# Kernel optimization log

Hardware: AMD Instinct MI355X
Metric: run time of the kernel (lower is better)

The kernel has to match this reference:

```python
import jax, jax.numpy as jnp
import numpy as np

B, M, E, K = 8, 256, 128, 16
H, A, R, RMS = 1024, 256, 1024, 512
NEG = -1e25


def setup_inputs() -> dict:
    key = jax.random.key(0)
    ks = jax.random.split(key, 12)
    inp = {
        "mention_reprs": jax.random.normal(ks[0], (B, M, H), jnp.float32),
        "entities": jax.random.randint(ks[1], (B, E, K), 0, M),
        "entity_masks": jax.random.randint(ks[2], (B, E, K), 0, 2, dtype=jnp.int32),
        "relation_memory": jax.random.normal(ks[3], (R, RMS), jnp.float32),
        # GatedMILAttention params
        "Wv": jax.random.normal(ks[4], (A, H), jnp.float32) / np.sqrt(H),
        "bv": jnp.zeros((A,), jnp.float32),
        "Wu": jax.random.normal(ks[5], (A, H), jnp.float32) / np.sqrt(H),
        "bu": jnp.zeros((A,), jnp.float32),
        "Wa": jax.random.normal(ks[6], (1, A), jnp.float32) / np.sqrt(A),
        "ba": jnp.zeros((1,), jnp.float32),
        # relation memory read linear: Linear(RMS, H)
        "Wr": jax.random.normal(ks[7], (H, RMS), jnp.float32) / np.sqrt(RMS),
        "br": jnp.zeros((H,), jnp.float32),
        # output linear: Linear(H + RMS, H)
        "Wo": jax.random.normal(ks[8], (H, H + RMS), jnp.float32) / np.sqrt(H + RMS),
        "bo": jnp.zeros((H,), jnp.float32),
    }
    return inp


def reference(mention_reprs, entities, entity_masks, relation_memory,
              Wv, bv, Wu, bu, Wa, ba, Wr, br, Wo, bo):
    # gather mention clusters: [B, E, K, H]
    clusters = jax.vmap(lambda m, e: m[e])(mention_reprs, entities)
    # gated MIL attention
    aV = jnp.tanh(jnp.einsum('bekh,ah->beka', clusters, Wv) + bv)
    aU = jax.nn.sigmoid(jnp.einsum('bekh,ah->beka', clusters, Wu) + bu)
    logits = jnp.einsum('beka,oa->beko', aV * aU, Wa) + ba  # [B,E,K,1]
    mask = entity_masks[..., None].astype(bool)
    logits = jnp.where(mask, logits, NEG)
    a = jax.nn.softmax(logits, axis=2)
    # weighted pooling over mentions: [B, E, H]
    entity_reprs = jnp.sum(a * clusters, axis=2)
    # relation memory read (memory detached for the read projection)
    s_w = jax.lax.stop_gradient(relation_memory) @ Wr.T + br        # [R, H]
    s = jnp.einsum('beh,rh->ber', entity_reprs, s_w)                # [B, E, R]
    s = jnp.einsum('ber,rm->bem', s, relation_memory)               # [B, E, RMS]
    out = jnp.concatenate([entity_reprs, s], axis=-1) @ Wo.T + bo   # [B, E, H]
    return out  # dropout is identity at inference
```

## Files before the change

### kernel.cpp

```cpp
#include <hip/hip_runtime.h>
#include <cstdint>
#include <cstddef>

#define NEG_ (-1e25f)

typedef __bf16 bf16x8 __attribute__((ext_vector_type(8)));
typedef float  f32x4  __attribute__((ext_vector_type(4)));
typedef short  s16x8  __attribute__((ext_vector_type(8)));
typedef const __attribute__((address_space(1))) void* gas_t;
typedef __attribute__((address_space(3))) void* las_t;

#define MFMA16 __builtin_amdgcn_mfma_f32_16x16x32_bf16

__device__ __forceinline__ short f2bf(float f) {
  union { float f; unsigned u; } v; v.f = f;
  unsigned r = v.u + 0x7fffu + ((v.u >> 16) & 1u);
  return (short)(r >> 16);
}

__device__ __forceinline__ s16x8 cvt8(const float* s) {
  bf16x8 r;
  #pragma unroll
  for (int j = 0; j < 8; ++j) r[j] = (__bf16)s[j];
  union { bf16x8 b; s16x8 s; } u; u.b = r; return u.s;
}

template <int NT>
__device__ void fgemm_dual(const float* __restrict__ A1, long lda1,
                           const float* __restrict__ A2, long lda2,
                           const float* __restrict__ B, long ldb,
                           short* __restrict__ C1, short* __restrict__ C2,
                           int ldc, int m0, int n0, short* lds) {
  const int tid = threadIdx.x, wave = tid >> 6, lane = tid & 63;
  const int quad = lane >> 4, l16 = lane & 15;
  const int wm = (wave & 1) * 32, wn = (wave >> 1) * 32;
  const int srow = tid >> 2, scol = (tid & 3) * 8;
  const float* A1g = A1 + (long)(m0 + srow) * lda1 + scol;
  const float* A2g = A2 + (long)(m0 + srow) * lda2 + scol;
  const float* Bg  = B  + (long)(n0 + srow) * ldb + scol;
  short* As1 = lds;
  short* As2 = lds + 2048;
  short* Bs  = lds + 4096;
  float r1[8], r2[8], rb[8];
  auto gload = [&](int kt) {
    long k = (long)kt * 32;
    *(float4*)(r1)     = *(const float4*)(A1g + k);
    *(float4*)(r1 + 4) = *(const float4*)(A1g + k + 4);
    *(float4*)(r2)     = *(const float4*)(A2g + k);
    *(float4*)(r2 + 4) = *(const float4*)(A2g + k + 4);
    *(float4*)(rb)     = *(const float4*)(Bg + k);
    *(float4*)(rb + 4) = *(const float4*)(Bg + k + 4);
  };
  f32x4 acc1[2][2] = {}, acc2[2][2] = {};
  gload(0);
  for (int kt = 0; kt < NT; ++kt) {
    *(s16x8*)&As1[srow * 32 + scol] = cvt8(r1);
    *(s16x8*)&As2[srow * 32 + scol] = cvt8(r2);
    *(s16x8*)&Bs[srow * 32 + scol]  = cvt8(rb);
    __syncthreads();
    if (kt + 1 < NT) gload(kt + 1);
    bf16x8 a10 = *(const bf16x8*)&As1[(wm + l16) * 32 + quad * 8];
    bf16x8 a11 = *(const bf16x8*)&As1[(wm + 16 + l16) * 32 + quad * 8];
    bf16x8 a20 = *(const bf16x8*)&As2[(wm + l16) * 32 + quad * 8];
    bf16x8 a21 = *(const bf16x8*)&As2[(wm + 16 + l16) * 32 + quad * 8];
    bf16x8 b0  = *(const bf16x8*)&Bs[(wn + l16) * 32 + quad * 8];
    bf16x8 b1  = *(const bf16x8*)&Bs[(wn + 16 + l16) * 32 + quad * 8];
    acc1[0][0] = MFMA16(a10, b0, acc1[0][0], 0, 0, 0);
    acc1[0][1] = MFMA16(a10, b1, acc1[0][1], 0, 0, 0);
    acc1[1][0] = MFMA16(a11, b0, acc1[1][0], 0, 0, 0);
    acc1[1][1] = MFMA16(a11, b1, acc1[1][1], 0, 0, 0);
    acc2[0][0] = MFMA16(a20, b0, acc2[0][0], 0, 0, 0);
    acc2[0][1] = MFMA16(a20, b1, acc2[0][1], 0, 0, 0);
    acc2[1][0] = MFMA16(a21, b0, acc2[1][0], 0, 0, 0);
    acc2[1][1] = MFMA16(a21, b1, acc2[1][1], 0, 0, 0);
    __syncthreads();
  }
  #pragma unroll
  for (int i = 0; i < 2; ++i)
    #pragma unroll
    for (int j = 0; j < 2; ++j) {
      int col = n0 + wn + j * 16 + l16;
      #pragma unroll
      for (int r = 0; r < 4; ++r) {
        int row = m0 + wm + i * 16 + quad * 4 + r;
        C1[(long)row * ldc + col] = f2bf(acc1[i][j][r]);
        C2[(long)row * ldc + col] = f2bf(acc2[i][j][r]);
      }
    }
}

template <int EPI>
__device__ void bgemm64(const short* __restrict__ A, int lda,
                        const short* __restrict__ B, int ldb,
                        void* __restrict__ C, int ldc, int NT, int m0, int n0,
                        const float* __restrict__ e0, const float* __restrict__ e1,
                        const float* __restrict__ e2, short* lds) {
  short* As = lds;
  short* Bs = lds + 4 * 2048;
  const int tid = threadIdx.x;
  const int wave = tid >> 6, lane = tid & 63;
  const int quad = lane >> 4, l16 = lane & 15;
  const int wm = (wave & 1) * 32, wn = (wave >> 1) * 32;
  const int srow = tid >> 2, scol = (tid & 3) * 8;
  const short* Ag = A + (long)(m0 + srow) * lda + scol;
  const short* Bg = B + (long)(n0 + srow) * ldb + scol;
  const int ldsoff = wave * 512;
  auto issue = [&](int kt) {
    int buf = kt & 3; int ko = kt * 32;
    __builtin_amdgcn_global_load_lds((gas_t)(Ag + ko), (las_t)(As + buf * 2048 + ldsoff), 16, 0, 0);
    __builtin_amdgcn_global_load_lds((gas_t)(Bg + ko), (las_t)(Bs + buf * 2048 + ldsoff), 16, 0, 0);
  };
  f32x4 acc[2][2] = {};
  issue(0); issue(1); issue(2);
  for (int kt = 0; kt < NT; ++kt) {
    int rem = NT - 1 - kt;
    if (rem >= 2)      asm volatile("s_waitcnt vmcnt(4)" ::: "memory");
    else if (rem == 1) asm volatile("s_waitcnt vmcnt(2)" ::: "memory");
    else               asm volatile("s_waitcnt vmcnt(0)" ::: "memory");
    asm volatile("s_barrier" ::: "memory");
    if (kt + 3 < NT) issue(kt + 3);
    const short* as = As + (kt & 3) * 2048;
    const short* bs = Bs + (kt & 3) * 2048;
    bf16x8 a0 = *(const bf16x8*)&as[(wm + l16) * 32 + quad * 8];
    bf16x8 a1 = *(const bf16x8*)&as[(wm + 16 + l16) * 32 + quad * 8];
    bf16x8 b0 = *(const bf16x8*)&bs[(wn + l16) * 32 + quad * 8];
    bf16x8 b1 = *(const bf16x8*)&bs[(wn + 16 + l16) * 32 + quad * 8];
    acc[0][0] = MFMA16(a0, b0, acc[0][0], 0, 0, 0);
    acc[0][1] = MFMA16(a0, b1, acc[0][1], 0, 0, 0);
    acc[1][0] = MFMA16(a1, b0, acc[1][0], 0, 0, 0);
    acc[1][1] = MFMA16(a1, b1, acc[1][1], 0, 0, 0);
  }
  #pragma unroll
  for (int i = 0; i < 2; ++i)
    #pragma unroll
    for (int j = 0; j < 2; ++j) {
      int col = n0 + wn + j * 16 + l16;
      #pragma unroll
      for (int r = 0; r < 4; ++r) {
        int row = m0 + wm + i * 16 + quad * 4 + r;
        float v = acc[i][j][r];
        if constexpr (EPI == 1) {
          v += e0[(long)row * 1536 + col];
          ((short*)C)[(long)row * ldc + col] = f2bf(v);
        } else {
          v += e0[col] + e1[row] * e2[col];
          ((float*)C)[(long)row * ldc + col] = v;
        }
      }
    }
}

__device__ void vu_tile(int mi, int ni, const float* __restrict__ X,
                        const float* __restrict__ Wv, const float* __restrict__ Wu,
                        const float* __restrict__ bv, const float* __restrict__ bu,
                        const float* __restrict__ Wa, float* __restrict__ wpart,
                        short* lds, float* red) {
  const int tid = threadIdx.x, wave = tid >> 6, lane = tid & 63;
  const int quad = lane >> 4, l16 = lane & 15;
  const int wm = (wave & 1) * 16, wn = (wave >> 1) * 32;
  const int m0 = mi * 32, n0 = ni * 64;
  const int srow = tid >> 2, scol = (tid & 3) * 8;
  short* As = lds;
  short* Bvs = lds + 1024;
  short* Bus = lds + 3072;
  const float* Ag  = X  + (long)(m0 + srow) * 1024 + scol;
  const float* Bvg = Wv + (long)(n0 + srow) * 1024 + scol;
  const float* Bug = Wu + (long)(n0 + srow) * 1024 + scol;
  float ra[8], rv[8], ru[8];
  auto gload = [&](int kt) {
    long k = (long)kt * 32;
    if (tid < 128) {
      *(float4*)(ra)     = *(const float4*)(Ag + k);
      *(float4*)(ra + 4) = *(const float4*)(Ag + k + 4);
    }
    *(float4*)(rv)     = *(const float4*)(Bvg + k);
    *(float4*)(rv + 4) = *(const float4*)(Bvg + k + 4);
    *(float4*)(ru)     = *(const float4*)(Bug + k);
    *(float4*)(ru + 4) = *(const float4*)(Bug + k + 4);
  };
  f32x4 accv[2] = {}, accu[2] = {};
  gload(0);
  for (int kt = 0; kt < 32; ++kt) {
    if (tid < 128) *(s16x8*)&As[srow * 32 + scol] = cvt8(ra);
    *(s16x8*)&Bvs[srow * 32 + scol] = cvt8(rv);
    *(s16x8*)&Bus[srow * 32 + scol] = cvt8(ru);
    __syncthreads();
    if (kt + 1 < 32) gload(kt + 1);
    bf16x8 af = *(const bf16x8*)&As[(wm + l16) * 32 + quad * 8];
    bf16x8 v0 = *(const bf16x8*)&Bvs[(wn + l16) * 32 + quad * 8];
    bf16x8 v1 = *(const bf16x8*)&Bvs[(wn + 16 + l16) * 32 + quad * 8];
    bf16x8 u0 = *(const bf16x8*)&Bus[(wn + l16) * 32 + quad * 8];
    bf16x8 u1 = *(const bf16x8*)&Bus[(wn + 16 + l16) * 32 + quad * 8];
    accv[0] = MFMA16(af, v0, accv[0], 0, 0, 0);
    accv[1] = MFMA16(af, v1, accv[1], 0, 0, 0);
    accu[0] = MFMA16(af, u0, accu[0], 0, 0, 0);
    accu[1] = MFMA16(af, u1, accu[1], 0, 0, 0);
    __syncthreads();
  }
  float wsum[4] = {0.f, 0.f, 0.f, 0.f};
  #pragma unroll
  for (int j = 0; j < 2; ++j) {
    int col = n0 + wn + j * 16 + l16;
    float bvc = bv[col], buc = bu[col], wac = Wa[col];
    #pragma unroll
    for (int r = 0; r < 4; ++r) {
      float vv = tanhf(accv[j][r] + bvc);
      float uu = accu[j][r] + buc;
      wsum[r] += (vv / (1.0f + expf(-uu))) * wac;
    }
  }
  #pragma unroll
  for (int r = 0; r < 4; ++r) {
    float s = wsum[r];
    s += __shfl_down(s, 8, 16);
    s += __shfl_down(s, 4, 16);
    s += __shfl_down(s, 2, 16);
    s += __shfl_down(s, 1, 16);
    if (l16 == 0) red[(wave >> 1) * 32 + wm + quad * 4 + r] = s;
  }
  __syncthreads();
  if (tid < 32) wpart[ni * 2048 + m0 + tid] = red[tid] + red[32 + tid];
}

__device__ void softmax_entity(int be, const float* __restrict__ ment,
    const int* __restrict__ ents, const int* __restrict__ msk,
    const float* __restrict__ wpart, const float* __restrict__ br,
    short* __restrict__ erb, float* __restrict__ cf,
    float* sm_a, int* sm_idx, float* sm_red) {
  const int b = be >> 7;
  const int tid = threadIdx.x;
  __syncthreads();
  if (tid < 16) {
    int idx = ents[be * 16 + tid];
    sm_idx[tid] = idx;
    int j = (b << 8) + idx;
    float lw = wpart[j] + wpart[2048 + j] + wpart[4096 + j] + wpart[6144 + j];
    sm_a[tid] = msk[be * 16 + tid] ? lw : NEG_;
  }
  __syncthreads();
  if (tid == 0) {
    float mx = sm_a[0];
    #pragma unroll
    for (int k = 1; k < 16; ++k) mx = fmaxf(mx, sm_a[k]);
    float e[16], s = 0.f;
    #pragma unroll
    for (int k = 0; k < 16; ++k) { e[k] = expf(sm_a[k] - mx); s += e[k]; }
    float inv = 1.0f / s;
    #pragma unroll
    for (int k = 0; k < 16; ++k) sm_a[k] = e[k] * inv;
  }
  __syncthreads();
  const float* Xr = ment + ((long)b << 18);
  const int h0 = tid * 4;
  float ax = 0.f, ay = 0.f, az = 0.f, aw = 0.f;
  #pragma unroll
  for (int k = 0; k < 16; ++k) {
    float ak = sm_a[k];
    float4 xv = *(const float4*)&Xr[(long)sm_idx[k] * 1024 + h0];
    ax += ak * xv.x; ay += ak * xv.y; az += ak * xv.z; aw += ak * xv.w;
  }
  short* er = erb + (long)be * 1024 + h0;
  er[0] = f2bf(ax); er[1] = f2bf(ay); er[2] = f2bf(az); er[3] = f2bf(aw);
  float4 brv = *(const float4*)&br[h0];
  float c = ax * brv.x + ay * brv.y + az * brv.z + aw * brv.w;
  #pragma unroll
  for (int off = 32; off > 0; off >>= 1) c += __shfl_down(c, off);
  if ((tid & 63) == 0) sm_red[tid >> 6] = c;
  __syncthreads();
  if (tid == 0) cf[be] = sm_red[0] + sm_red[1] + sm_red[2] + sm_red[3];
}

__global__ __launch_bounds__(256) void k1(
    const float* __restrict__ rm, const float* __restrict__ ment,
    const float* __restrict__ Wv, const float* __restrict__ Wu,
    const float* __restrict__ bv, const float* __restrict__ bu,
    const float* __restrict__ Wa, const float* __restrict__ Wr,
    const float* __restrict__ Wo, short* __restrict__ swTb,
    short* __restrict__ Ub, float* __restrict__ wpart) {
  __shared__ short lds[6144];
  __shared__ float red[64];
  const int blk = blockIdx.x;
  if (blk < 256) {
    fgemm_dual<16>(Wr, 512, Wo + 1024, 1536, rm, 512, swTb, Ub, 1024,
                   (blk >> 4) * 64, (blk & 15) * 64, lds);
  } else {
    int q = blk - 256;
    vu_tile(q & 63, q >> 6, ment, Wv, Wu, bv, bu, Wa, wpart, lds, red);
  }
}

__global__ __launch_bounds__(256) void k2(
    const short* __restrict__ Ub, const short* __restrict__ swTb,
    const float* __restrict__ Wo, const float* __restrict__ ment,
    const int* __restrict__ ents, const int* __restrict__ msk,
    const float* __restrict__ wpart, const float* __restrict__ br,
    short* __restrict__ Weffb, float* __restrict__ gw2,
    short* __restrict__ erb, float* __restrict__ cf) {
  __shared__ short lds[16384];
  __shared__ float sm_a[16];
  __shared__ int   sm_idx[16];
  __shared__ float sm_red[4];
  const int blk = blockIdx.x, tid = threadIdx.x;
  if (blk < 256) {
    bgemm64<1>(Ub, 1024, swTb, 1024, Weffb, 1024, 32,
               (blk >> 4) * 64, (blk & 15) * 64, Wo, nullptr, nullptr, lds);
  } else if (blk < 260) {
    int row = (blk - 256) * 256 + tid;
    const short* u = Ub + (long)row * 1024;
    float s = 0.f;
    for (int k = 0; k < 1024; k += 8) {
      s16x8 v = *(const s16x8*)&u[k];
      union { s16x8 s; bf16x8 b; } w; w.s = v;
      #pragma unroll
      for (int j = 0; j < 8; ++j) s += (float)w.b[j];
    }
    gw2[row] = s;
  } else {
    int s4 = (blk - 260) * 4;
    for (int e = 0; e < 4; ++e)
      softmax_entity(s4 + e, ment, ents, msk, wpart, br, erb, cf,
                     sm_a, sm_idx, sm_red);
  }
}

__global__ __launch_bounds__(256) void k3(
    const short* __restrict__ erb, const short* __restrict__ Weffb,
    const float* __restrict__ bo, const float* __restrict__ cf,
    const float* __restrict__ gw2, float* __restrict__ out) {
  __shared__ short lds[16384];
  const int blk = blockIdx.x;
  bgemm64<2>(erb, 1024, Weffb, 1024, out, 1024, 32,
             (blk >> 4) * 64, (blk & 15) * 64, bo, cf, gw2, lds);
}

extern "C" void kernel_launch(void* const* d_in, const int* in_sizes, int n_in,
                              void* d_out, int out_size, void* d_ws, size_t ws_size,
                              hipStream_t stream) {
  const float* ment = (const float*)d_in[0];
  const int*   ents = (const int*)d_in[1];
  const int*   msk  = (const int*)d_in[2];
  const float* rm   = (const float*)d_in[3];
  const float* Wv   = (const float*)d_in[4];
  const float* bv   = (const float*)d_in[5];
  const float* Wu   = (const float*)d_in[6];
  const float* bu   = (const float*)d_in[7];
  const float* Wa   = (const float*)d_in[8];
  const float* Wr   = (const float*)d_in[10];
  const float* br   = (const float*)d_in[11];
  const float* Wo   = (const float*)d_in[12];
  const float* bo   = (const float*)d_in[13];
  float* out = (float*)d_out;

  char* p = (char*)d_ws;
  auto alloc = [&](size_t bytes) {
    void* q = (void*)p; p += (bytes + 255) & ~(size_t)255; return q;
  };
  short* swTb  = (short*)alloc((size_t)1024 * 1024 * 2);
  short* Ub    = (short*)alloc((size_t)1024 * 1024 * 2);
  short* Weffb = (short*)alloc((size_t)1024 * 1024 * 2);
  short* erb   = (short*)alloc((size_t)1024 * 1024 * 2);
  float* wpart = (float*)alloc((size_t)4 * 2048 * 4);
  float* cf    = (float*)alloc((size_t)1024 * 4);
  float* gw2   = (float*)alloc((size_t)1024 * 4);

  k1<<<512, 256, 0, stream>>>(rm, ment, Wv, Wu, bv, bu, Wa, Wr, Wo,
                              swTb, Ub, wpart);
  k2<<<516, 256, 0, stream>>>(Ub, swTb, Wo, ment, ents, msk, wpart, br,
                              Weffb, gw2, erb, cf);
  k3<<<256, 256, 0, stream>>>(erb, Weffb, bo, cf, gw2, out);
}
```

Baseline: 141.7 us.

## Pre-convert inputs to bf16 and pipeline k1 GEMMs with async LDS ring

Adds a k0 pass that converts the mention, Wv, Wu, rm, Wr and the Wo slice from fp32 to bf16 once. The k1 dual GEMM and the V/U gating GEMM then load bf16 tiles directly into a 4-deep LDS ring with global_load_lds, using vmcnt waits instead of register staging and two barriers per step. The entity softmax/pooling and the gw2 row sums in k2 are rewritten as one wave per entity using shuffles instead of block-wide shared-memory syncs. This costs an extra launch and extra global traffic for the converted copies, in exchange for halving bytes in the GEMM loops and overlapping loads with MFMA.

```diff
diff --git a/kernel.cpp b/kernel.cpp
--- a/kernel.cpp
+++ b/kernel.cpp
@@ -25,46 +25,76 @@
   union { bf16x8 b; s16x8 s; } u; u.b = r; return u.s;
 }
 
-template <int NT>
-__device__ void fgemm_dual(const float* __restrict__ A1, long lda1,
-                           const float* __restrict__ A2, long lda2,
-                           const float* __restrict__ B, long ldb,
-                           short* __restrict__ C1, short* __restrict__ C2,
-                           int ldc, int m0, int n0, short* lds) {
+struct Params {
+  const float* ment; const int* ents; const int* msk;
+  const float* rm; const float* Wv; const float* bv; const float* Wu;
+  const float* bu; const float* Wa; const float* Wr; const float* br;
+  const float* Wo; const float* bo; float* out;
+  short *Xb, *Wvb, *Wub, *rmb, *Wrb, *Wo2b, *swTb, *Ub, *Weffb, *erb;
+  float *wpart, *cf, *gw2;
+};
+
+__global__ __launch_bounds__(256) void k0(Params p) {
+  const int g = blockIdx.x * 256 + threadIdx.x;
+  #pragma unroll
+  for (int it = 0; it < 4; ++it) {
+    int u = g + it * 131072;
+    long e = (long)u * 8;
+    const float* src; short* dst;
+    if (u < 262144)      { src = p.ment + e;                     dst = p.Xb + e; }
+    else if (u < 294912) { long o = e - 2097152; src = p.Wv + o; dst = p.Wvb + o; }
+    else if (u < 327680) { long o = e - 2359296; src = p.Wu + o; dst = p.Wub + o; }
+    else if (u < 393216) { long o = e - 2621440; src = p.rm + o; dst = p.rmb + o; }
+    else if (u < 458752) { long o = e - 3145728; src = p.Wr + o; dst = p.Wrb + o; }
+    else                 { long o = e - 3670016;
+                           src = p.Wo + (o >> 9) * 1536 + 1024 + (o & 511);
+                           dst = p.Wo2b + o; }
+    float t[8];
+    *(float4*)t       = *(const float4*)src;
+    *(float4*)(t + 4) = *(const float4*)(src + 4);
+    *(s16x8*)dst = cvt8(t);
+  }
+}
+
+__device__ void bgemm_dual(const short* __restrict__ A1, const short* __restrict__ A2,
+                           long lda, const short* __restrict__ B, long ldb,
+                           short* __restrict__ C1, short* __restrict__ C2, int ldc,
+                           int NT, int m0, int n0, short* lds) {
+  short* As1 = lds;
+  short* As2 = lds + 4 * 2048;
+  short* Bs  = lds + 8 * 2048;
   const int tid = threadIdx.x, wave = tid >> 6, lane = tid & 63;
   const int quad = lane >> 4, l16 = lane & 15;
   const int wm = (wave & 1) * 32, wn = (wave >> 1) * 32;
   const int srow = tid >> 2, scol = (tid & 3) * 8;
-  const float* A1g = A1 + (long)(m0 + srow) * lda1 + scol;
-  const float* A2g = A2 + (long)(m0 + srow) * lda2 + scol;
-  const float* Bg  = B  + (long)(n0 + srow) * ldb + scol;
-  short* As1 = lds;
-  short* As2 = lds + 2048;
-  short* Bs  = lds + 4096;
-  float r1[8], r2[8], rb[8];
-  auto gload = [&](int kt) {
-    long k = (long)kt * 32;
-    *(float4*)(r1)     = *(const float4*)(A1g + k);
-    *(float4*)(r1 + 4) = *(const float4*)(A1g + k + 4);
-    *(float4*)(r2)     = *(const float4*)(A2g + k);
-    *(float4*)(r2 + 4) = *(const float4*)(A2g + k + 4);
-    *(float4*)(rb)     = *(const float4*)(Bg + k);
-    *(float4*)(rb + 4) = *(const float4*)(Bg + k + 4);
+  const short* A1g = A1 + (long)(m0 + srow) * lda + scol;
+  const short* A2g = A2 + (long)(m0 + srow) * lda + scol;
+  const short* Bg  = B  + (long)(n0 + srow) * ldb + scol;
+  const int ldsoff = wave * 512;
+  auto issue = [&](int kt) {
+    int buf = kt & 3; int ko = kt * 32;
+    __builtin_amdgcn_global_load_lds((gas_t)(A1g + ko), (las_t)(As1 + buf * 2048 + ldsoff), 16, 0, 0);
+    __builtin_amdgcn_global_load_lds((gas_t)(A2g + ko), (las_t)(As2 + buf * 2048 + ldsoff), 16, 0, 0);
+    __builtin_amdgcn_global_load_lds((gas_t)(Bg  + ko), (las_t)(Bs  + buf * 2048 + ldsoff), 16, 0, 0);
   };
   f32x4 acc1[2][2] = {}, acc2[2][2] = {};
-  gload(0);
+  issue(0); issue(1); issue(2);
   for (int kt = 0; kt < NT; ++kt) {
-    *(s16x8*)&As1[srow * 32 + scol] = cvt8(r1);
-    *(s16x8*)&As2[srow * 32 + scol] = cvt8(r2);
-    *(s16x8*)&Bs[srow * 32 + scol]  = cvt8(rb);
-    __syncthreads();
-    if (kt + 1 < NT) gload(kt + 1);
-    bf16x8 a10 = *(const bf16x8*)&As1[(wm + l16) * 32 + quad * 8];
-    bf16x8 a11 = *(const bf16x8*)&As1[(wm + 16 + l16) * 32 + quad * 8];
-    bf16x8 a20 = *(const bf16x8*)&As2[(wm + l16) * 32 + quad * 8];
-    bf16x8 a21 = *(const bf16x8*)&As2[(wm + 16 + l16) * 32 + quad * 8];
-    bf16x8 b0  = *(const bf16x8*)&Bs[(wn + l16) * 32 + quad * 8];
-    bf16x8 b1  = *(const bf16x8*)&Bs[(wn + 16 + l16) * 32 + quad * 8];
+    int rem = NT - 1 - kt;
+    if (rem >= 2)      asm volatile("s_waitcnt vmcnt(6)" ::: "memory");
+    else if (rem == 1) asm volatile("s_waitcnt vmcnt(3)" ::: "memory");
+    else               asm volatile("s_waitcnt vmcnt(0)" ::: "memory");
+    asm volatile("s_barrier" ::: "memory");
+    if (kt + 3 < NT) issue(kt + 3);
+    const short* as1 = As1 + (kt & 3) * 2048;
+    const short* as2 = As2 + (kt & 3) * 2048;
+    const short* bs  = Bs  + (kt & 3) * 2048;
+    bf16x8 a10 = *(const bf16x8*)&as1[(wm + l16) * 32 + quad * 8];
+    bf16x8 a11 = *(const bf16x8*)&as1[(wm + 16 + l16) * 32 + quad * 8];
+    bf16x8 a20 = *(const bf16x8*)&as2[(wm + l16) * 32 + quad * 8];
+    bf16x8 a21 = *(const bf16x8*)&as2[(wm + 16 + l16) * 32 + quad * 8];
+    bf16x8 b0  = *(const bf16x8*)&bs[(wn + l16) * 32 + quad * 8];
+    bf16x8 b1  = *(const bf16x8*)&bs[(wn + 16 + l16) * 32 + quad * 8];
     acc1[0][0] = MFMA16(a10, b0, acc1[0][0], 0, 0, 0);
     acc1[0][1] = MFMA16(a10, b1, acc1[0][1], 0, 0, 0);
     acc1[1][0] = MFMA16(a11, b0, acc1[1][0], 0, 0, 0);
@@ -73,7 +103,6 @@
     acc2[0][1] = MFMA16(a20, b1, acc2[0][1], 0, 0, 0);
     acc2[1][0] = MFMA16(a21, b0, acc2[1][0], 0, 0, 0);
     acc2[1][1] = MFMA16(a21, b1, acc2[1][1], 0, 0, 0);
-    __syncthreads();
   }
   #pragma unroll
   for (int i = 0; i < 2; ++i)
@@ -150,58 +179,59 @@
     }
 }
 
-__device__ void vu_tile(int mi, int ni, const float* __restrict__ X,
-                        const float* __restrict__ Wv, const float* __restrict__ Wu,
-                        const float* __restrict__ bv, const float* __restrict__ bu,
-                        const float* __restrict__ Wa, float* __restrict__ wpart,
-                        short* lds, float* red) {
+__device__ void vu_ring(int mi, int ni, const Params& p, short* lds, float* red) {
+  short* As  = lds;
+  short* Bvs = lds + 4 * 1024;
+  short* Bus = lds + 4 * 1024 + 4 * 2048;
   const int tid = threadIdx.x, wave = tid >> 6, lane = tid & 63;
   const int quad = lane >> 4, l16 = lane & 15;
   const int wm = (wave & 1) * 16, wn = (wave >> 1) * 32;
   const int m0 = mi * 32, n0 = ni * 64;
   const int srow = tid >> 2, scol = (tid & 3) * 8;
-  short* As = lds;
-  short* Bvs = lds + 1024;
-  short* Bus = lds + 3072;
-  const float* Ag  = X  + (long)(m0 + srow) * 1024 + scol;
-  const float* Bvg = Wv + (long)(n0 + srow) * 1024 + scol;
-  const float* Bug = Wu + (long)(n0 + srow) * 1024 + scol;
-  float ra[8], rv[8], ru[8];
-  auto gload = [&](int kt) {
-    long k = (long)kt * 32;
-    if (tid < 128) {
-      *(float4*)(ra)     = *(const float4*)(Ag + k);
-      *(float4*)(ra + 4) = *(const float4*)(Ag + k + 4);
-    }
-    *(float4*)(rv)     = *(const float4*)(Bvg + k);
-    *(float4*)(rv + 4) = *(const float4*)(Bvg + k + 4);
-    *(float4*)(ru)     = *(const float4*)(Bug + k);
-    *(float4*)(ru + 4) = *(const float4*)(Bug + k + 4);
+  const short* Ag  = p.Xb  + (long)(m0 + srow) * 1024 + scol;
+  const short* Bvg = p.Wvb + (long)(n0 + srow) * 1024 + scol;
+  const short* Bug = p.Wub + (long)(n0 + srow) * 1024 + scol;
+  const int ldsoff = wave * 512;
+  auto issue = [&](int kt) {
+    int buf = kt & 3; int ko = kt * 32;
+    if (wave < 2)
+      __builtin_amdgcn_global_load_lds((gas_t)(Ag + ko), (las_t)(As + buf * 1024 + ldsoff), 16, 0, 0);
+    __builtin_amdgcn_global_load_lds((gas_t)(Bvg + ko), (las_t)(Bvs + buf * 2048 + ldsoff), 16, 0, 0);
+    __builtin_amdgcn_global_load_lds((gas_t)(Bug + ko), (las_t)(Bus + buf * 2048 + ldsoff), 16, 0, 0);
   };
   f32x4 accv[2] = {}, accu[2] = {};
-  gload(0);
+  issue(0); issue(1); issue(2);
   for (int kt = 0; kt < 32; ++kt) {
-    if (tid < 128) *(s16x8*)&As[srow * 32 + scol] = cvt8(ra);
-    *(s16x8*)&Bvs[srow * 32 + scol] = cvt8(rv);
-    *(s16x8*)&Bus[srow * 32 + scol] = cvt8(ru);
-    __syncthreads();
-    if (kt + 1 < 32) gload(kt + 1);
-    bf16x8 af = *(const bf16x8*)&As[(wm + l16) * 32 + quad * 8];
-    bf16x8 v0 = *(const bf16x8*)&Bvs[(wn + l16) * 32 + quad * 8];
-    bf16x8 v1 = *(const bf16x8*)&Bvs[(wn + 16 + l16) * 32 + quad * 8];
-    bf16x8 u0 = *(const bf16x8*)&Bus[(wn + l16) * 32 + quad * 8];
-    bf16x8 u1 = *(const bf16x8*)&Bus[(wn + 16 + l16) * 32 + quad * 8];
+    int rem = 31 - kt;
+    if (wave < 2) {
+      if (rem >= 2)      asm volatile("s_waitcnt vmcnt(6)" ::: "memory");
+      else if (rem == 1) asm volatile("s_waitcnt vmcnt(3)" ::: "memory");
+      else               asm volatile("s_waitcnt vmcnt(0)" ::: "memory");
+    } else {
+      if (rem >= 2)      asm volatile("s_waitcnt vmcnt(4)" ::: "memory");
+      else if (rem == 1) asm volatile("s_waitcnt vmcnt(2)" ::: "memory");
+      else               asm volatile("s_waitcnt vmcnt(0)" ::: "memory");
+    }
+    asm volatile("s_barrier" ::: "memory");
+    if (kt + 3 < 32) issue(kt + 3);
+    const short* as  = As  + (kt & 3) * 1024;
+    const short* bvs = Bvs + (kt & 3) * 2048;
+    const short* bus = Bus + (kt & 3) * 2048;
+    bf16x8 af = *(const bf16x8*)&as[(wm + l16) * 32 + quad * 8];
+    bf16x8 v0 = *(const bf16x8*)&bvs[(wn + l16) * 32 + quad * 8];
+    bf16x8 v1 = *(const bf16x8*)&bvs[(wn + 16 + l16) * 32 + quad * 8];
+    bf16x8 u0 = *(const bf16x8*)&bus[(wn + l16) * 32 + quad * 8];
+    bf16x8 u1 = *(const bf16x8*)&bus[(wn + 16 + l16) * 32 + quad * 8];
     accv[0] = MFMA16(af, v0, accv[0], 0, 0, 0);
     accv[1] = MFMA16(af, v1, accv[1], 0, 0, 0);
     accu[0] = MFMA16(af, u0, accu[0], 0, 0, 0);
     accu[1] = MFMA16(af, u1, accu[1], 0, 0, 0);
-    __syncthreads();
   }
   float wsum[4] = {0.f, 0.f, 0.f, 0.f};
   #pragma unroll
   for (int j = 0; j < 2; ++j) {
     int col = n0 + wn + j * 16 + l16;
-    float bvc = bv[col], buc = bu[col], wac = Wa[col];
+    float bvc = p.bv[col], buc = p.bu[col], wac = p.Wa[col];
     #pragma unroll
     for (int r = 0; r < 4; ++r) {
       float vv = tanhf(accv[j][r] + bvc);
@@ -219,153 +249,153 @@
     if (l16 == 0) red[(wave >> 1) * 32 + wm + quad * 4 + r] = s;
   }
   __syncthreads();
-  if (tid < 32) wpart[ni * 2048 + m0 + tid] = red[tid] + red[32 + tid];
-}
-
-__device__ void softmax_entity(int be, const float* __restrict__ ment,
-    const int* __restrict__ ents, const int* __restrict__ msk,
-    const float* __restrict__ wpart, const float* __restrict__ br,
-    short* __restrict__ erb, float* __restrict__ cf,
-    float* sm_a, int* sm_idx, float* sm_red) {
+  if (tid < 32) p.wpart[ni * 2048 + m0 + tid] = red[tid] + red[32 + tid];
+}
+
+__device__ void gw2_wave(int row, const Params& p) {
+  const int lane = threadIdx.x & 63;
+  const short* u = p.Ub + (long)row * 1024 + lane * 16;
+  union { s16x8 s; bf16x8 b; } w0, w1;
+  w0.s = *(const s16x8*)u;
+  w1.s = *(const s16x8*)(u + 8);
+  float s = 0.f;
+  #pragma unroll
+  for (int j = 0; j < 8; ++j) s += (float)w0.b[j] + (float)w1.b[j];
+  #pragma unroll
+  for (int off = 32; off > 0; off >>= 1) s += __shfl_down(s, off);
+  if (lane == 0) p.gw2[row] = s;
+}
+
+__device__ void entity_wave(int be, const Params& p) {
+  const int lane = threadIdx.x & 63;
   const int b = be >> 7;
-  const int tid = threadIdx.x;
-  __syncthreads();
-  if (tid < 16) {
-    int idx = ents[be * 16 + tid];
-    sm_idx[tid] = idx;
+  float a = NEG_; int idx = 0;
+  if (lane < 16) {
+    idx = p.ents[be * 16 + lane];
     int j = (b << 8) + idx;
-    float lw = wpart[j] + wpart[2048 + j] + wpart[4096 + j] + wpart[6144 + j];
-    sm_a[tid] = msk[be * 16 + tid] ? lw : NEG_;
-  }
-  __syncthreads();
-  if (tid == 0) {
-    float mx = sm_a[0];
+    float lw = p.wpart[j] + p.wpart[2048 + j] + p.wpart[4096 + j] + p.wpart[6144 + j];
+    a = p.msk[be * 16 + lane] ? lw : NEG_;
+  }
+  float m = a;
+  m = fmaxf(m, __shfl_xor(m, 1, 16));
+  m = fmaxf(m, __shfl_xor(m, 2, 16));
+  m = fmaxf(m, __shfl_xor(m, 4, 16));
+  m = fmaxf(m, __shfl_xor(m, 8, 16));
+  float e = expf(a - m);
+  float s = e;
+  s += __shfl_xor(s, 1, 16);
+  s += __shfl_xor(s, 2, 16);
+  s += __shfl_xor(s, 4, 16);
+  s += __shfl_xor(s, 8, 16);
+  float aw = e / s;
+  const float* Xr = p.ment + ((long)b << 18);
+  const int h0 = lane * 16;
+  float acc[16];
+  #pragma unroll
+  for (int t = 0; t < 16; ++t) acc[t] = 0.f;
+  #pragma unroll
+  for (int k = 0; k < 16; ++k) {
+    float ak = __shfl(aw, k);
+    int   ik = __shfl(idx, k);
+    const float* xr = Xr + (long)ik * 1024 + h0;
+    f32x4 x0 = *(const f32x4*)(xr);
+    f32x4 x1 = *(const f32x4*)(xr + 4);
+    f32x4 x2 = *(const f32x4*)(xr + 8);
+    f32x4 x3 = *(const f32x4*)(xr + 12);
     #pragma unroll
-    for (int k = 1; k < 16; ++k) mx = fmaxf(mx, sm_a[k]);
-    float e[16], s = 0.f;
-    #pragma unroll
-    for (int k = 0; k < 16; ++k) { e[k] = expf(sm_a[k] - mx); s += e[k]; }
-    float inv = 1.0f / s;
-    #pragma unroll
-    for (int k = 0; k < 16; ++k) sm_a[k] = e[k] * inv;
-  }
-  __syncthreads();
-  const float* Xr = ment + ((long)b << 18);
-  const int h0 = tid * 4;
-  float ax = 0.f, ay = 0.f, az = 0.f, aw = 0.f;
-  #pragma unroll
-  for (int k = 0; k < 16; ++k) {
-    float ak = sm_a[k];
-    float4 xv = *(const float4*)&Xr[(long)sm_idx[k] * 1024 + h0];
-    ax += ak * xv.x; ay += ak * xv.y; az += ak * xv.z; aw += ak * xv.w;
-  }
-  short* er = erb + (long)be * 1024 + h0;
-  er[0] = f2bf(ax); er[1] = f2bf(ay); er[2] = f2bf(az); er[3] = f2bf(aw);
-  float4 brv = *(const float4*)&br[h0];
-  float c = ax * brv.x + ay * brv.y + az * brv.z + aw * brv.w;
+    for (int t = 0; t < 4; ++t) {
+      acc[t]      += ak * x0[t];
+      acc[4 + t]  += ak * x1[t];
+      acc[8 + t]  += ak * x2[t];
+      acc[12 + t] += ak * x3[t];
+    }
+  }
+  short* er = p.erb + (long)be * 1024 + h0;
+  *(s16x8*)er       = cvt8(acc);
+  *(s16x8*)(er + 8) = cvt8(acc + 8);
+  float c = 0.f;
+  const float* brp = p.br + h0;
+  #pragma unroll
+  for (int t = 0; t < 16; ++t) c += acc[t] * brp[t];
   #pragma unroll
   for (int off = 32; off > 0; off >>= 1) c += __shfl_down(c, off);
-  if ((tid & 63) == 0) sm_red[tid >> 6] = c;
-  __syncthreads();
-  if (tid == 0) cf[be] = sm_red[0] + sm_red[1] + sm_red[2] + sm_red[3];
-}
-
-__global__ __launch_bounds__(256) void k1(
-    const float* __restrict__ rm, const float* __restrict__ ment,
-    const float* __restrict__ Wv, const float* __restrict__ Wu,
-    const float* __restrict__ bv, const float* __restrict__ bu,
-    const float* __restrict__ Wa, const float* __restrict__ Wr,
-    const float* __restrict__ Wo, short* __restrict__ swTb,
-    short* __restrict__ Ub, float* __restrict__ wpart) {
-  __shared__ short lds[6144];
+  if (lane == 0) p.cf[be] = c;
+}
+
+__global__ __launch_bounds__(256) void k1(Params p) {
+  __shared__ short lds[24576];
   __shared__ float red[64];
   const int blk = blockIdx.x;
   if (blk < 256) {
-    fgemm_dual<16>(Wr, 512, Wo + 1024, 1536, rm, 512, swTb, Ub, 1024,
-                   (blk >> 4) * 64, (blk & 15) * 64, lds);
+    bgemm_dual(p.Wrb, p.Wo2b, 512, p.rmb, 512, p.swTb, p.Ub, 1024, 16,
+               (blk >> 4) * 64, (blk & 15) * 64, lds);
   } else {
     int q = blk - 256;
-    vu_tile(q & 63, q >> 6, ment, Wv, Wu, bv, bu, Wa, wpart, lds, red);
-  }
-}
-
-__global__ __launch_bounds__(256) void k2(
-    const short* __restrict__ Ub, const short* __restrict__ swTb,
-    const float* __restrict__ Wo, const float* __restrict__ ment,
-    const int* __restrict__ ents, const int* __restrict__ msk,
-    const float* __restrict__ wpart, const float* __restrict__ br,
-    short* __restrict__ Weffb, float* __restrict__ gw2,
-    short* __restrict__ erb, float* __restrict__ cf) {
-  __shared__ short lds[16384];
-  __shared__ float sm_a[16];
-  __shared__ int   sm_idx[16];
-  __shared__ float sm_red[4];
-  const int blk = blockIdx.x, tid = threadIdx.x;
-  if (blk < 256) {
-    bgemm64<1>(Ub, 1024, swTb, 1024, Weffb, 1024, 32,
-               (blk >> 4) * 64, (blk & 15) * 64, Wo, nullptr, nullptr, lds);
-  } else if (blk < 260) {
-    int row = (blk - 256) * 256 + tid;
-    const short* u = Ub + (long)row * 1024;
-    float s = 0.f;
-    for (int k = 0; k < 1024; k += 8) {
-      s16x8 v = *(const s16x8*)&u[k];
-      union { s16x8 s; bf16x8 b; } w; w.s = v;
-      #pragma unroll
-      for (int j = 0; j < 8; ++j) s += (float)w.b[j];
-    }
-    gw2[row] = s;
-  } else {
-    int s4 = (blk - 260) * 4;
-    for (int e = 0; e < 4; ++e)
-      softmax_entity(s4 + e, ment, ents, msk, wpart, br, erb, cf,
-                     sm_a, sm_idx, sm_red);
-  }
-}
-
-__global__ __launch_bounds__(256) void k3(
-    const short* __restrict__ erb, const short* __restrict__ Weffb,
-    const float* __restrict__ bo, const float* __restrict__ cf,
-    const float* __restrict__ gw2, float* __restrict__ out) {
+    vu_ring(q & 63, q >> 6, p, lds, red);
+  }
+}
+
+__global__ __launch_bounds__(256) void k2(Params p) {
   __shared__ short lds[16384];
   const int blk = blockIdx.x;
-  bgemm64<2>(erb, 1024, Weffb, 1024, out, 1024, 32,
-             (blk >> 4) * 64, (blk & 15) * 64, bo, cf, gw2, lds);
+  if (blk < 256) {
+    bgemm64<1>(p.Ub, 1024, p.swTb, 1024, p.Weffb, 1024, 32,
+               (blk >> 4) * 64, (blk & 15) * 64, p.Wo, nullptr, nullptr, lds);
+  } else {
+    int q = blk - 256;
+    int wave = threadIdx.x >> 6;
+    gw2_wave(q * 4 + wave, p);
+    entity_wave(q * 4 + wave, p);
+  }
+}
+
+__global__ __launch_bounds__(256) void k3(Params p) {
+  __shared__ short lds[16384];
+  const int blk = blockIdx.x;
+  bgemm64<2>(p.erb, 1024, p.Weffb, 1024, p.out, 1024, 32,
+             (blk >> 4) * 64, (blk & 15) * 64, p.bo, p.cf, p.gw2, lds);
 }
 
 extern "C" void kernel_launch(void* const* d_in, const int* in_sizes, int n_in,
                               void* d_out, int out_size, void* d_ws, size_t ws_size,
                               hipStream_t stream) {
-  const float* ment = (const float*)d_in[0];
-  const int*   ents = (const int*)d_in[1];
-  const int*   msk  = (const int*)d_in[2];
-  const float* rm   = (const float*)d_in[3];
-  const float* Wv   = (const float*)d_in[4];
-  const float* bv   = (const float*)d_in[5];
-  const float* Wu   = (const float*)d_in[6];
-  const float* bu   = (const float*)d_in[7];
-  const float* Wa   = (const float*)d_in[8];
-  const float* Wr   = (const float*)d_in[10];
-  const float* br   = (const float*)d_in[11];
-  const float* Wo   = (const float*)d_in[12];
-  const float* bo   = (const float*)d_in[13];
-  float* out = (float*)d_out;
-
-  char* p = (char*)d_ws;
+  (void)in_sizes; (void)n_in; (void)out_size; (void)ws_size;
+  Params p;
+  p.ment = (const float*)d_in[0];
+  p.ents = (const int*)d_in[1];
+  p.msk  = (const int*)d_in[2];
+  p.rm   = (const float*)d_in[3];
+  p.Wv   = (const float*)d_in[4];
+  p.bv   = (const float*)d_in[5];
+  p.Wu   = (const float*)d_in[6];
+  p.bu   = (const float*)d_in[7];
+  p.Wa   = (const float*)d_in[8];
+  p.Wr   = (const float*)d_in[10];
+  p.br   = (const float*)d_in[11];
+  p.Wo   = (const float*)d_in[12];
+  p.bo   = (const float*)d_in[13];
+  p.out  = (float*)d_out;
+
+  char* w = (char*)d_ws;
   auto alloc = [&](size_t bytes) {
-    void* q = (void*)p; p += (bytes + 255) & ~(size_t)255; return q;
+    void* q = (void*)w; w += (bytes + 255) & ~(size_t)255; return q;
   };
-  short* swTb  = (short*)alloc((size_t)1024 * 1024 * 2);
-  short* Ub    = (short*)alloc((size_t)1024 * 1024 * 2);
-  short* Weffb = (short*)alloc((size_t)1024 * 1024 * 2);
-  short* erb   = (short*)alloc((size_t)1024 * 1024 * 2);
-  float* wpart = (float*)alloc((size_t)4 * 2048 * 4);
-  float* cf    = (float*)alloc((size_t)1024 * 4);
-  float* gw2   = (float*)alloc((size_t)1024 * 4);
-
-  k1<<<512, 256, 0, stream>>>(rm, ment, Wv, Wu, bv, bu, Wa, Wr, Wo,
-                              swTb, Ub, wpart);
-  k2<<<516, 256, 0, stream>>>(Ub, swTb, Wo, ment, ents, msk, wpart, br,
-                              Weffb, gw2, erb, cf);
-  k3<<<256, 256, 0, stream>>>(erb, Weffb, bo, cf, gw2, out);
-}
+  p.Xb    = (short*)alloc((size_t)2048 * 1024 * 2);
+  p.Wvb   = (short*)alloc((size_t)256 * 1024 * 2);
+  p.Wub   = (short*)alloc((size_t)256 * 1024 * 2);
+  p.rmb   = (short*)alloc((size_t)1024 * 512 * 2);
+  p.Wrb   = (short*)alloc((size_t)1024 * 512 * 2);
+  p.Wo2b  = (short*)alloc((size_t)1024 * 512 * 2);
+  p.swTb  = (short*)alloc((size_t)1024 * 1024 * 2);
+  p.Ub    = (short*)alloc((size_t)1024 * 1024 * 2);
+  p.Weffb = (short*)alloc((size_t)1024 * 1024 * 2);
+  p.erb   = (short*)alloc((size_t)1024 * 1024 * 2);
+  p.wpart = (float*)alloc((size_t)4 * 2048 * 4);
+  p.cf    = (float*)alloc((size_t)1024 * 4);
+  p.gw2   = (float*)alloc((size_t)1024 * 4);
+
+  k0<<<512, 256, 0, stream>>>(p);
+  k1<<<512, 256, 0, stream>>>(p);
+  k2<<<512, 256, 0, stream>>>(p);
+  k3<<<256, 256, 0, stream>>>(p);
+}
```

Result: faster. 138.2 us (-2.5%).
